# Kernel tuning notes

Hardware: AMD Instinct MI355X
Metric: run time of the kernel (lower is better)

The kernel has to match this reference:

```python
import jax, jax.numpy as jnp
import numpy as np

NUM_IMGS = 16
MASKS_PER_IMG = 8   # masks per image (one annotation group per image)
REGION_TOKENS = 4   # region_token_num


def setup_inputs() -> dict:
    key = jax.random.key(0)
    k1, k2, k3, k4, k5, k6 = jax.random.split(key, 6)
    C_in, C_hid = 1024, 4096
    feats = jax.random.normal(k1, (NUM_IMGS * MASKS_PER_IMG, 576, C_in), jnp.float32)
    masks = jax.random.normal(k2, (NUM_IMGS, MASKS_PER_IMG, 336, 336), jnp.float32)
    W1 = jax.random.normal(k3, (C_in, C_hid), jnp.float32) * (1.0 / np.sqrt(C_in))
    b1 = jax.random.normal(k4, (C_hid,), jnp.float32) * 0.02
    W2 = jax.random.normal(k5, (C_hid, C_hid), jnp.float32) * (1.0 / np.sqrt(C_hid))
    b2 = jax.random.normal(k6, (C_hid,), jnp.float32) * 0.02
    return {"feats": feats, "masks": masks, "W1": W1, "b1": b1, "W2": W2, "b2": b2}


def _token_merge(x, r, num_out):
    # x: [n, d]; merge contiguous runs of high-similarity tokens down to num_out tokens
    nrm = x / jnp.maximum(jnp.linalg.norm(x, axis=-1, keepdims=True), 1e-12)
    sim = jnp.sum(nrm[:-1] * nrm[1:], axis=-1)          # [n-1]
    vals, _ = jax.lax.top_k(sim, r)
    kth = vals[-1]                                      # r-th largest similarity
    cut = (sim < kth).astype(jnp.int32)                 # boundary after token i
    seg = jnp.concatenate([jnp.zeros((1,), jnp.int32), jnp.cumsum(cut)])  # [n]
    sums = jax.ops.segment_sum(x, seg, num_segments=num_out)
    counts = jax.ops.segment_sum(jnp.ones((x.shape[0],), x.dtype), seg, num_segments=num_out)
    return sums / jnp.maximum(counts, 1.0)[:, None]     # [num_out, d]


def reference(feats, masks, W1, b1, W2, b2):
    num_imgs, M, H, W = masks.shape
    P, C = feats.shape[1], feats.shape[2]
    N = int(round(P ** 0.5))                            # 24
    feats_g = feats.reshape(num_imgs, M, N, N, C)       # grouped per image

    def per_image(feat, mask):
        # feat: [M, N, N, C], mask: [M, H, W]
        m = jax.image.resize(mask, (M, N, N), method="bilinear")  # align_corners=False semantics
        m = (m > 0).astype(feat.dtype)
        denorm = m.sum(axis=(-1, -2)) + 1e-8            # [M]
        pooled = jnp.einsum("mijc,mij->mc", feat, m) / denorm[:, None]  # [M, C]
        return _token_merge(pooled, M - REGION_TOKENS, REGION_TOKENS)    # [R, C]

    merged = jax.vmap(per_image)(feats_g, masks)        # [num_imgs, R, C]
    tokens = merged.reshape(-1, C)                      # [num_imgs*R, C]
    h = jax.nn.gelu(tokens @ W1 + b1, approximate=False)
    return h @ W2 + b2
```

## Files before the change

kernel.cpp:

```cpp
#include <hip/hip_runtime.h>
#include <hip/hip_bf16.h>
#include <math.h>

#define NIMG 16
#define MPI  8
#define NPAIR 128
#define RTOK 4
#define HW_  336
#define NN_  24
#define P_   576
#define C_   1024
#define CH_  4096
#define NTOK 64
#define TAPS 28
#define PSLICE 8
#define S1 16
#define S2 16

__device__ __forceinline__ int wstart(int o){ int s = 14*o - 7; return s < 0 ? 0 : s; }

__global__ __launch_bounds__(256) void k_resizeW(const float* __restrict__ masks,
                                                 float* __restrict__ Tg) {
  int gsz = gridDim.x * 256;
  for (int idx = blockIdx.x*256 + threadIdx.x; idx < NPAIR*HW_*NN_; idx += gsz) {
    int oc = idx % NN_;
    int rowIdx = idx / NN_;
    const float* row = masks + (size_t)rowIdx * HW_;
    int st = wstart(oc);
    float s_o = 14.0f*(float)oc + 6.5f;
    float wt[TAPS];
    float wsum = 0.f;
    #pragma unroll
    for (int t = 0; t < TAPS; t++) {
      int p = st + t;
      float w = (p < HW_) ? fmaxf(0.f, 1.f - fabsf((float)p - s_o)*(1.0f/14.0f)) : 0.f;
      wt[t] = w; wsum += w;
    }
    float inv = 1.0f / wsum;
    float s = 0.f;
    #pragma unroll
    for (int t = 0; t < TAPS; t++) {
      int p = st + t; p = (p < HW_) ? p : (HW_-1);
      s += (wt[t]*inv) * row[p];
    }
    Tg[idx] = s;
  }
}

__global__ __launch_bounds__(256) void k_resizeH(const float* __restrict__ Tg,
                                                 unsigned short* __restrict__ actIdx,
                                                 int* __restrict__ cnt) {
  int pair = blockIdx.x;
  int tid = threadIdx.x;
  __shared__ float T[HW_*NN_];
  __shared__ int lcnt;
  const float4* src = (const float4*)(Tg + (size_t)pair*HW_*NN_);
  float4* dst = (float4*)T;
  for (int i = tid; i < HW_*NN_/4; i += 256) dst[i] = src[i];
  if (tid == 0) lcnt = 0;
  __syncthreads();

  for (int idx = tid; idx < P_; idx += 256) {
    int oh = idx / NN_, ow = idx % NN_;
    int st = wstart(oh);
    float s_o = 14.0f*(float)oh + 6.5f;
    float wt[TAPS];
    float wsum = 0.f;
    #pragma unroll
    for (int t = 0; t < TAPS; t++) {
      int r = st + t;
      float w = (r < HW_) ? fmaxf(0.f, 1.f - fabsf((float)r - s_o)*(1.0f/14.0f)) : 0.f;
      wt[t] = w; wsum += w;
    }
    float inv = 1.0f / wsum;
    float s = 0.f;
    #pragma unroll
    for (int t = 0; t < TAPS; t++) {
      int r = st + t; r = (r < HW_) ? r : (HW_-1);
      s += (wt[t]*inv) * T[r*NN_ + ow];
    }
    if (s > 0.f) {
      int pos = atomicAdd(&lcnt, 1);
      actIdx[(size_t)pair*P_ + pos] = (unsigned short)idx;
    }
  }
  __syncthreads();
  if (tid == 0) cnt[pair] = lcnt;
}

__global__ __launch_bounds__(256) void k_pool(const float* __restrict__ feats,
                                              const unsigned short* __restrict__ actIdx,
                                              const int* __restrict__ cnt,
                                              float* __restrict__ poolPart) {
  int slice = blockIdx.x & (PSLICE-1);
  int pair  = blockIdx.x / PSLICE;
  int n  = cnt[pair];
  int lo = (n * slice) / PSLICE;
  int hi = (n * (slice+1)) / PSLICE;
  int tid = threadIdx.x;
  const unsigned short* ai = actIdx + (size_t)pair*P_;
  const float* fb = feats + (size_t)pair * P_ * C_ + 4*tid;
  float4 acc = make_float4(0.f, 0.f, 0.f, 0.f);
  int i = lo;
  for (; i + 8 <= hi; i += 8) {
    int r0 = ai[i+0], r1 = ai[i+1], r2 = ai[i+2], r3 = ai[i+3];
    int r4 = ai[i+4], r5 = ai[i+5], r6 = ai[i+6], r7 = ai[i+7];
    float4 v0 = *(const float4*)(fb + (size_t)r0*C_);
    float4 v1 = *(const float4*)(fb + (size_t)r1*C_);
    float4 v2 = *(const float4*)(fb + (size_t)r2*C_);
    float4 v3 = *(const float4*)(fb + (size_t)r3*C_);
    float4 v4 = *(const float4*)(fb + (size_t)r4*C_);
    float4 v5 = *(const float4*)(fb + (size_t)r5*C_);
    float4 v6 = *(const float4*)(fb + (size_t)r6*C_);
    float4 v7 = *(const float4*)(fb + (size_t)r7*C_);
    acc.x += v0.x; acc.y += v0.y; acc.z += v0.z; acc.w += v0.w;
    acc.x += v1.x; acc.y += v1.y; acc.z += v1.z; acc.w += v1.w;
    acc.x += v2.x; acc.y += v2.y; acc.z += v2.z; acc.w += v2.w;
    acc.x += v3.x; acc.y += v3.y; acc.z += v3.z; acc.w += v3.w;
    acc.x += v4.x; acc.y += v4.y; acc.z += v4.z; acc.w += v4.w;
    acc.x += v5.x; acc.y += v5.y; acc.z += v5.z; acc.w += v5.w;
    acc.x += v6.x; acc.y += v6.y; acc.z += v6.z; acc.w += v6.w;
    acc.x += v7.x; acc.y += v7.y; acc.z += v7.z; acc.w += v7.w;
  }
  for (; i < hi; i++) {
    const float4 v = *(const float4*)(fb + (size_t)ai[i]*C_);
    acc.x += v.x; acc.y += v.y; acc.z += v.z; acc.w += v.w;
  }
  *(float4*)(poolPart + ((size_t)slice*NPAIR + pair)*C_ + 4*tid) = acc;
}

__global__ __launch_bounds__(256) void k_merge(const float* __restrict__ poolPart,
                                               const int* __restrict__ cnt,
                                               float* __restrict__ tokT) {
  int img = blockIdx.x;
  int tid = threadIdx.x;
  int wv = tid >> 6, ln = tid & 63;
  __shared__ float pool[MPI][C_];
  __shared__ float nrm[MPI][C_];
  __shared__ float norms[MPI];
  __shared__ float sims[MPI];
  __shared__ int seg[MPI];

  for (int idx = tid; idx < MPI*C_/4; idx += 256) {
    int m_ = idx >> 8, q = idx & 255;
    int pair = img*MPI + m_;
    float4 s = make_float4(0.f,0.f,0.f,0.f);
    #pragma unroll
    for (int sl = 0; sl < PSLICE; sl++) {
      float4 v = *(const float4*)(poolPart + ((size_t)sl*NPAIR + pair)*C_ + q*4);
      s.x += v.x; s.y += v.y; s.z += v.z; s.w += v.w;
    }
    float inv = 1.0f / ((float)cnt[pair] + 1e-8f);
    pool[m_][q*4+0] = s.x * inv; pool[m_][q*4+1] = s.y * inv;
    pool[m_][q*4+2] = s.z * inv; pool[m_][q*4+3] = s.w * inv;
  }
  __syncthreads();

  for (int h = 0; h < 2; h++) {
    int m_ = wv*2 + h;
    float s = 0.f;
    for (int c = ln; c < C_; c += 64) { float v = pool[m_][c]; s += v*v; }
    for (int o = 32; o > 0; o >>= 1) s += __shfl_xor(s, o);
    if (ln == 0) norms[m_] = fmaxf(sqrtf(s), 1e-12f);
  }
  __syncthreads();

  for (int idx = tid; idx < MPI*C_; idx += 256) {
    int m_ = idx >> 10, c = idx & (C_-1);
    nrm[m_][c] = pool[m_][c] / norms[m_];
  }
  __syncthreads();

  for (int h = 0; h < 2; h++) {
    int i = wv + h*4;
    if (i < MPI-1) {
      float s = 0.f;
      for (int c = ln; c < C_; c += 64) s += nrm[i][c]*nrm[i+1][c];
      for (int o = 32; o > 0; o >>= 1) s += __shfl_xor(s, o);
      if (ln == 0) sims[i] = s;
    }
  }
  __syncthreads();

  if (tid == 0) {
    float v[MPI-1];
    for (int i = 0; i < MPI-1; i++) v[i] = sims[i];
    for (int i = 1; i < MPI-1; i++) {
      float key = v[i]; int j = i-1;
      while (j >= 0 && v[j] < key) { v[j+1] = v[j]; j--; }
      v[j+1] = key;
    }
    float kth = v[RTOK-1];
    int s = 0; seg[0] = 0;
    for (int i = 1; i < MPI; i++) { if (sims[i-1] < kth) s++; seg[i] = s; }
  }
  __syncthreads();

  for (int idx = tid; idx < RTOK*C_; idx += 256) {
    int r = idx >> 10, c = idx & (C_-1);
    float s = 0.f; int k = 0;
    #pragma unroll
    for (int m_ = 0; m_ < MPI; m_++) {
      if (seg[m_] == r) { s += pool[m_][c]; k++; }
    }
    tokT[(size_t)c*NTOK + img*RTOK + r] = s / fmaxf((float)k, 1.0f);
  }
}

#define FMA4(ACC,AV) ACC.x=fmaf(AV,w.x,ACC.x);ACC.y=fmaf(AV,w.y,ACC.y);ACC.z=fmaf(AV,w.z,ACC.z);ACC.w=fmaf(AV,w.w,ACC.w)
__global__ __launch_bounds__(64) void k_gemm(const float* __restrict__ AT,
                                             const float* __restrict__ W,
                                             float* __restrict__ part,
                                             int N, int KS) {
  int ln = threadIdx.x;
  int mi = ln >> 4;
  int ji = ln & 15;
  int jc = blockIdx.x*64 + ji*4;
  int k0 = blockIdx.y*KS;
  float4 acc[16];
  #pragma unroll
  for (int r = 0; r < 16; r++) acc[r] = make_float4(0.f,0.f,0.f,0.f);

  const float* ap    = AT + (size_t)k0*NTOK + mi*16;
  const float* wbase = W  + (size_t)k0*N + jc;
  const float* wp    = wbase;
  float4 wbuf[8];
  #pragma unroll
  for (int kk = 0; kk < 8; kk++) wbuf[kk] = *(const float4*)(wp + (size_t)kk*N);
  wp += 8*(size_t)N;

  for (int k8 = 0; k8 < KS; k8 += 8) {
    bool more = (k8 + 8) < KS;
    const float* pre = more ? wp : wbase;
    #pragma unroll
    for (int kk = 0; kk < 8; kk++) {
      float4 a0 = *(const float4*)(ap);
      float4 a1 = *(const float4*)(ap+4);
      float4 a2 = *(const float4*)(ap+8);
      float4 a3 = *(const float4*)(ap+12);
      ap += NTOK;
      float4 w = wbuf[kk];
      FMA4(acc[0], a0.x); FMA4(acc[1], a0.y); FMA4(acc[2], a0.z); FMA4(acc[3], a0.w);
      FMA4(acc[4], a1.x); FMA4(acc[5], a1.y); FMA4(acc[6], a1.z); FMA4(acc[7], a1.w);
      FMA4(acc[8], a2.x); FMA4(acc[9], a2.y); FMA4(acc[10],a2.z); FMA4(acc[11],a2.w);
      FMA4(acc[12],a3.x); FMA4(acc[13],a3.y); FMA4(acc[14],a3.z); FMA4(acc[15],a3.w);
      wbuf[kk] = *(const float4*)(pre + (size_t)kk*N);
    }
    wp += 8*(size_t)N;
  }
  #pragma unroll
  for (int q = 0; q < 4; q++)
    #pragma unroll
    for (int r = 0; r < 4; r++) {
      int row = mi*16 + q*4 + r;
      *(float4*)(part + ((size_t)blockIdx.y*NTOK + row)*N + jc) = acc[q*4+r];
    }
}

__global__ __launch_bounds__(256) void k_reduce1(const float* __restrict__ part,
                                                 const float* __restrict__ b1,
                                                 float* __restrict__ hT) {
  __shared__ float tile[64][65];
  int j0 = blockIdx.x * 64;
  int tid = threadIdx.x;
  for (int i = tid; i < 64*64; i += 256) {
    int m = i >> 6, jj = i & 63;
    float s = 0.f;
    #pragma unroll
    for (int ss = 0; ss < S1; ss++) s += part[((size_t)ss*NTOK + m)*CH_ + j0 + jj];
    s += b1[j0 + jj];
    float g = 0.5f * s * (1.0f + erff(s * 0.70710678118654752f));
    tile[jj][m] = g;
  }
  __syncthreads();
  for (int i = tid; i < 64*64; i += 256) {
    int jj = i >> 6, m = i & 63;
    hT[(size_t)(j0 + jj)*NTOK + m] = tile[jj][m];
  }
}

__global__ __launch_bounds__(256) void k_reduce2(const float* __restrict__ part,
                                                 const float* __restrict__ b2,
                                                 float* __restrict__ out) {
  int idx = blockIdx.x*256 + threadIdx.x;
  float s = 0.f;
  #pragma unroll
  for (int ss = 0; ss < S2; ss++) s += part[(size_t)ss*NTOK*CH_ + idx];
  out[idx] = s + b2[idx & (CH_-1)];
}

extern "C" void kernel_launch(void* const* d_in, const int* in_sizes, int n_in,
                              void* d_out, int out_size, void* d_ws, size_t ws_size,
                              hipStream_t stream) {
  (void)in_sizes; (void)n_in; (void)out_size; (void)ws_size;
  const float* feats = (const float*)d_in[0];
  const float* masks = (const float*)d_in[1];
  const float* W1    = (const float*)d_in[2];
  const float* b1    = (const float*)d_in[3];
  const float* W2    = (const float*)d_in[4];
  const float* b2    = (const float*)d_in[5];
  float* out = (float*)d_out;
  char* ws = (char*)d_ws;

  unsigned short* actIdx = (unsigned short*)(ws + 0);
  int*   cnt      = (int*)  (ws + 147456);
  float* Tg       = (float*)(ws + 147968);
  float* poolPart = (float*)(ws + 4276736);
  float* tokT     = (float*)(ws + 8471040);
  float* g1part   = (float*)(ws + 8733184);
  float* hT       = (float*)(ws + 25510400);
  float* g2part   = (float*)(ws + 26558976);

  k_resizeW<<<1024, 256, 0, stream>>>(masks, Tg);
  k_resizeH<<<NPAIR, 256, 0, stream>>>(Tg, actIdx, cnt);
  k_pool <<<NPAIR*PSLICE, 256, 0, stream>>>(feats, actIdx, cnt, poolPart);
  k_merge<<<NIMG, 256, 0, stream>>>(poolPart, cnt, tokT);
  k_gemm <<<dim3(CH_/64, S1), 64, 0, stream>>>(tokT, W1, g1part, CH_, C_/S1);
  k_reduce1<<<CH_/64, 256, 0, stream>>>(g1part, b1, hT);
  k_gemm <<<dim3(CH_/64, S2), 64, 0, stream>>>(hT, W2, g2part, CH_, CH_/S2);
  k_reduce2<<<(NTOK*CH_)/256, 256, 0, stream>>>(g2part, b2, out);
}
```

Before: 666.3 us.

## Fuse mask resize passes into one kernel and vectorize partial-sum reductions

Result: no change. 663.7 us (-0.4%).

```diff
diff --git a/kernel.cpp b/kernel.cpp
--- a/kernel.cpp
+++ b/kernel.cpp
@@ -13,71 +13,65 @@
 #define CH_  4096
 #define NTOK 64
 #define TAPS 28
+#define TAPS_P 29
 #define PSLICE 8
 #define S1 16
 #define S2 16
 
 __device__ __forceinline__ int wstart(int o){ int s = 14*o - 7; return s < 0 ? 0 : s; }
 
-__global__ __launch_bounds__(256) void k_resizeW(const float* __restrict__ masks,
-                                                 float* __restrict__ Tg) {
-  int gsz = gridDim.x * 256;
-  for (int idx = blockIdx.x*256 + threadIdx.x; idx < NPAIR*HW_*NN_; idx += gsz) {
-    int oc = idx % NN_;
-    int rowIdx = idx / NN_;
-    const float* row = masks + (size_t)rowIdx * HW_;
-    int st = wstart(oc);
-    float s_o = 14.0f*(float)oc + 6.5f;
-    float wt[TAPS];
-    float wsum = 0.f;
+__global__ __launch_bounds__(512) void k_mask(const float* __restrict__ masks,
+                                              unsigned short* __restrict__ actIdx,
+                                              int* __restrict__ cnt) {
+  int pair = blockIdx.x;
+  const float* gm = masks + (size_t)pair * (HW_*HW_);
+  __shared__ float wW[NN_][TAPS_P];
+  __shared__ float T[HW_*NN_];
+  __shared__ int lcnt;
+  int tid = threadIdx.x;
+
+  if (tid < NN_) {
+    int o = tid;
+    int st = wstart(o);
+    float s_o = 14.0f*(float)o + 6.5f;
+    float tmp[TAPS];
+    float sum = 0.f;
     #pragma unroll
     for (int t = 0; t < TAPS; t++) {
       int p = st + t;
       float w = (p < HW_) ? fmaxf(0.f, 1.f - fabsf((float)p - s_o)*(1.0f/14.0f)) : 0.f;
-      wt[t] = w; wsum += w;
-    }
-    float inv = 1.0f / wsum;
+      tmp[t] = w; sum += w;
+    }
+    float inv = 1.0f / sum;
+    #pragma unroll
+    for (int t = 0; t < TAPS; t++) wW[o][t] = tmp[t]*inv;
+  }
+  if (tid == 0) lcnt = 0;
+  __syncthreads();
+
+  for (int idx = tid; idx < HW_*NN_; idx += 512) {
+    int oc = idx % NN_;
+    int r  = idx / NN_;
+    const float* row = gm + (size_t)r*HW_;
+    int st = wstart(oc);
     float s = 0.f;
     #pragma unroll
     for (int t = 0; t < TAPS; t++) {
       int p = st + t; p = (p < HW_) ? p : (HW_-1);
-      s += (wt[t]*inv) * row[p];
-    }
-    Tg[idx] = s;
-  }
-}
-
-__global__ __launch_bounds__(256) void k_resizeH(const float* __restrict__ Tg,
-                                                 unsigned short* __restrict__ actIdx,
-                                                 int* __restrict__ cnt) {
-  int pair = blockIdx.x;
-  int tid = threadIdx.x;
-  __shared__ float T[HW_*NN_];
-  __shared__ int lcnt;
-  const float4* src = (const float4*)(Tg + (size_t)pair*HW_*NN_);
-  float4* dst = (float4*)T;
-  for (int i = tid; i < HW_*NN_/4; i += 256) dst[i] = src[i];
-  if (tid == 0) lcnt = 0;
-  __syncthreads();
-
-  for (int idx = tid; idx < P_; idx += 256) {
+      s += wW[oc][t] * row[p];
+    }
+    T[idx] = s;
+  }
+  __syncthreads();
+
+  for (int idx = tid; idx < P_; idx += 512) {
     int oh = idx / NN_, ow = idx % NN_;
     int st = wstart(oh);
-    float s_o = 14.0f*(float)oh + 6.5f;
-    float wt[TAPS];
-    float wsum = 0.f;
-    #pragma unroll
-    for (int t = 0; t < TAPS; t++) {
-      int r = st + t;
-      float w = (r < HW_) ? fmaxf(0.f, 1.f - fabsf((float)r - s_o)*(1.0f/14.0f)) : 0.f;
-      wt[t] = w; wsum += w;
-    }
-    float inv = 1.0f / wsum;
     float s = 0.f;
     #pragma unroll
     for (int t = 0; t < TAPS; t++) {
       int r = st + t; r = (r < HW_) ? r : (HW_-1);
-      s += (wt[t]*inv) * T[r*NN_ + ow];
+      s += wW[oh][t] * T[r*NN_ + ow];
     }
     if (s > 0.f) {
       int pos = atomicAdd(&lcnt, 1);
@@ -263,14 +257,20 @@
   __shared__ float tile[64][65];
   int j0 = blockIdx.x * 64;
   int tid = threadIdx.x;
-  for (int i = tid; i < 64*64; i += 256) {
-    int m = i >> 6, jj = i & 63;
-    float s = 0.f;
-    #pragma unroll
-    for (int ss = 0; ss < S1; ss++) s += part[((size_t)ss*NTOK + m)*CH_ + j0 + jj];
-    s += b1[j0 + jj];
-    float g = 0.5f * s * (1.0f + erff(s * 0.70710678118654752f));
-    tile[jj][m] = g;
+  for (int i = tid; i < 64*16; i += 256) {
+    int m = i >> 4, jq = i & 15;
+    float4 s = make_float4(0.f,0.f,0.f,0.f);
+    #pragma unroll
+    for (int ss = 0; ss < S1; ss++) {
+      float4 v = *(const float4*)(part + ((size_t)ss*NTOK + m)*CH_ + j0 + jq*4);
+      s.x += v.x; s.y += v.y; s.z += v.z; s.w += v.w;
+    }
+    float4 b = *(const float4*)(b1 + j0 + jq*4);
+    s.x += b.x; s.y += b.y; s.z += b.z; s.w += b.w;
+    tile[jq*4+0][m] = 0.5f*s.x*(1.0f + erff(s.x*0.70710678118654752f));
+    tile[jq*4+1][m] = 0.5f*s.y*(1.0f + erff(s.y*0.70710678118654752f));
+    tile[jq*4+2][m] = 0.5f*s.z*(1.0f + erff(s.z*0.70710678118654752f));
+    tile[jq*4+3][m] = 0.5f*s.w*(1.0f + erff(s.w*0.70710678118654752f));
   }
   __syncthreads();
   for (int i = tid; i < 64*64; i += 256) {
@@ -279,14 +279,19 @@
   }
 }
 
-__global__ __launch_bounds__(256) void k_reduce2(const float* __restrict__ part,
-                                                 const float* __restrict__ b2,
-                                                 float* __restrict__ out) {
+__global__ __launch_bounds__(256) void k_reduce2(const float4* __restrict__ part,
+                                                 const float4* __restrict__ b2,
+                                                 float4* __restrict__ out) {
   int idx = blockIdx.x*256 + threadIdx.x;
-  float s = 0.f;
+  float4 s = make_float4(0.f,0.f,0.f,0.f);
   #pragma unroll
-  for (int ss = 0; ss < S2; ss++) s += part[(size_t)ss*NTOK*CH_ + idx];
-  out[idx] = s + b2[idx & (CH_-1)];
+  for (int ss = 0; ss < S2; ss++) {
+    float4 v = part[(size_t)ss*(NTOK*CH_/4) + idx];
+    s.x += v.x; s.y += v.y; s.z += v.z; s.w += v.w;
+  }
+  float4 b = b2[idx & (CH_/4 - 1)];
+  s.x += b.x; s.y += b.y; s.z += b.z; s.w += b.w;
+  out[idx] = s;
 }
 
 extern "C" void kernel_launch(void* const* d_in, const int* in_sizes, int n_in,
@@ -304,19 +309,17 @@
 
   unsigned short* actIdx = (unsigned short*)(ws + 0);
   int*   cnt      = (int*)  (ws + 147456);
-  float* Tg       = (float*)(ws + 147968);
-  float* poolPart = (float*)(ws + 4276736);
-  float* tokT     = (float*)(ws + 8471040);
-  float* g1part   = (float*)(ws + 8733184);
-  float* hT       = (float*)(ws + 25510400);
-  float* g2part   = (float*)(ws + 26558976);
-
-  k_resizeW<<<1024, 256, 0, stream>>>(masks, Tg);
-  k_resizeH<<<NPAIR, 256, 0, stream>>>(Tg, actIdx, cnt);
+  float* poolPart = (float*)(ws + 147968);
+  float* tokT     = (float*)(ws + 4342272);
+  float* g1part   = (float*)(ws + 4604416);
+  float* hT       = (float*)(ws + 21381632);
+  float* g2part   = (float*)(ws + 22430208);
+
+  k_mask <<<NPAIR, 512, 0, stream>>>(masks, actIdx, cnt);
   k_pool <<<NPAIR*PSLICE, 256, 0, stream>>>(feats, actIdx, cnt, poolPart);
   k_merge<<<NIMG, 256, 0, stream>>>(poolPart, cnt, tokT);
   k_gemm <<<dim3(CH_/64, S1), 64, 0, stream>>>(tokT, W1, g1part, CH_, C_/S1);
   k_reduce1<<<CH_/64, 256, 0, stream>>>(g1part, b1, hT);
   k_gemm <<<dim3(CH_/64, S2), 64, 0, stream>>>(hT, W2, g2part, CH_, CH_/S2);
-  k_reduce2<<<(NTOK*CH_)/256, 256, 0, stream>>>(g2part, b2, out);
-}
+  k_reduce2<<<(NTOK*CH_/4)/256, 256, 0, stream>>>((const float4*)g2part, (const float4*)b2, (float4*)out);
+}
```
